# Kernel tuning notes

Hardware: AMD Instinct MI355X
Metric: run time of the kernel (lower is better)

## Reference

```python
import jax, jax.numpy as jnp
import numpy as np

D = 1024      # n_embedding
H = 16        # n_head
DH = D // H   # head_size = 64
T = 2048      # block_size / seq len
B = 2
EPS = 1e-5


def layer_norm(x, gamma, beta):
    mu = jnp.mean(x, axis=-1, keepdims=True)
    var = jnp.mean((x - mu) ** 2, axis=-1, keepdims=True)
    return (x - mu) * jax.lax.rsqrt(var + EPS) * gamma + beta


def setup_inputs() -> dict:
    key = jax.random.key(0)
    ks = jax.random.split(key, 12)
    s = 0.02
    return {
        "x": jax.random.normal(ks[0], (B, T, D), jnp.float32),
        # per-head QKV projections stacked over heads: [H, D, DH] (no bias, as in Head)
        "wq": jax.random.normal(ks[1], (H, D, DH), jnp.float32) * s,
        "wk": jax.random.normal(ks[2], (H, D, DH), jnp.float32) * s,
        "wv": jax.random.normal(ks[3], (H, D, DH), jnp.float32) * s,
        # output projection [H*DH, D] with bias
        "w_proj": jax.random.normal(ks[4], (H * DH, D), jnp.float32) * s,
        "b_proj": jnp.zeros((D,), jnp.float32),
        # feedforward: D -> 4D -> D
        "w1": jax.random.normal(ks[5], (D, 4 * D), jnp.float32) * s,
        "b1": jnp.zeros((4 * D,), jnp.float32),
        "w2": jax.random.normal(ks[6], (4 * D, D), jnp.float32) * s,
        "b2": jnp.zeros((D,), jnp.float32),
        # layer norms
        "ln1_g": jnp.ones((D,), jnp.float32),
        "ln1_b": jnp.zeros((D,), jnp.float32),
        "ln2_g": jnp.ones((D,), jnp.float32),
        "ln2_b": jnp.zeros((D,), jnp.float32),
    }


def reference(x, wq, wk, wv, w_proj, b_proj, w1, b1, w2, b2,
              ln1_g, ln1_b, ln2_g, ln2_b):
    # pre-LN attention sub-block
    xn = layer_norm(x, ln1_g, ln1_b)                      # [B,T,D]
    q = jnp.einsum('btd,hdk->bhtk', xn, wq)               # [B,H,T,DH]
    k = jnp.einsum('btd,hdk->bhtk', xn, wk)
    v = jnp.einsum('btd,hdk->bhtk', xn, wv)
    scale = DH ** -0.5
    scores = jnp.einsum('bhtk,bhsk->bhts', q, k) * scale  # [B,H,T,T]
    causal = jnp.tril(jnp.ones((T, T), bool))
    scores = jnp.where(causal, scores, -jnp.inf)
    attn = jax.nn.softmax(scores, axis=-1)
    out = jnp.einsum('bhts,bhsk->bhtk', attn, v)          # [B,H,T,DH]
    out = out.transpose(0, 2, 1, 3).reshape(B, T, H * DH)  # concat heads
    x = x + out @ w_proj + b_proj                          # residual 1
    # pre-LN feedforward sub-block
    xn2 = layer_norm(x, ln2_g, ln2_b)
    h = jax.nn.relu(xn2 @ w1 + b1)
    x = x + h @ w2 + b2                                    # residual 2
    return x
```

## Files before the change

### kernel.cpp

```cpp
#include <hip/hip_runtime.h>
#include <hip/hip_bf16.h>
#include <math.h>


#define D_MODEL 1024
#define NH 16
#define DHEAD 64
#define SEQ 2048
#define NTOK 4096

typedef __bf16 bf16x8 __attribute__((ext_vector_type(8)));
typedef float f32x4 __attribute__((ext_vector_type(4)));
typedef float f32x16 __attribute__((ext_vector_type(16)));
typedef unsigned short u16x8 __attribute__((ext_vector_type(8)));

__device__ __forceinline__ unsigned short f2b(float f) {
  unsigned u = __builtin_bit_cast(unsigned, f);
  u = u + 0x7fffu + ((u >> 16) & 1u);
  return (unsigned short)(u >> 16);
}

__device__ __forceinline__ bf16x8 ld_bf16x8(const unsigned short* p) {
  u16x8 u = *(const u16x8*)p;
  return __builtin_bit_cast(bf16x8, u);
}

__device__ __forceinline__ void async16(void* lds, const void* g) {
  __builtin_amdgcn_global_load_lds(
      (const __attribute__((address_space(1))) unsigned int*)g,
      (__attribute__((address_space(3))) unsigned int*)lds, 16, 0, 0);
}

__device__ __forceinline__ bf16x8 ds_read16(const void* p) {
  bf16x8 r;
  unsigned a = (unsigned)(size_t)(const __attribute__((address_space(3))) void*)p;
  asm volatile("ds_read_b128 %0, %1" : "=v"(r) : "v"(a));
  return r;
}
__device__ __forceinline__ void ds_write32(void* p, unsigned v) {
  unsigned a = (unsigned)(size_t)(__attribute__((address_space(3))) void*)p;
  asm volatile("ds_write_b32 %0, %1" :: "v"(a), "v"(v));
}
__device__ __forceinline__ unsigned cvt_pk_bf16(float lo, float hi) {
  unsigned d;
  asm("v_cvt_pk_bf16_f32 %0, %1, %2" : "=v"(d) : "v"(lo), "v"(hi));
  return d;
}
#define WAIT_LGKM0_FENCE() do { \
  asm volatile("s_waitcnt lgkmcnt(0)" ::: "memory"); \
  __builtin_amdgcn_sched_barrier(0); } while (0)
#define WAIT_LGKM8_FENCE() do { \
  asm volatile("s_waitcnt lgkmcnt(8)" ::: "memory"); \
  __builtin_amdgcn_sched_barrier(0); } while (0)

__global__ __launch_bounds__(256) void prep_fused(
    const float* __restrict__ wq, const float* __restrict__ wk,
    const float* __restrict__ wv, const float* __restrict__ w_proj,
    const float* __restrict__ w1, const float* __restrict__ w2,
    const float* __restrict__ x, const float* __restrict__ ln1g,
    const float* __restrict__ ln1b,
    unsigned short* __restrict__ WqkvT, unsigned short* __restrict__ wprojT,
    unsigned short* __restrict__ w1T, unsigned short* __restrict__ w2T,
    unsigned short* __restrict__ xn) {
  __shared__ float tile[64][65];
  __shared__ float ps[4], ps2[4];
  const int bid = blockIdx.x;
  const int tidx = threadIdx.x;

  if (bid < 3072) {
    const float* in;
    unsigned short* outp;
    int r0, c0, R, C;
    if (bid < 768) {
      int t = bid;
      int sel = t >> 8, hh = (t >> 4) & 15, rt = t & 15;
      in = (sel == 0 ? wq : sel == 1 ? wk : wv) + (size_t)hh * D_MODEL * DHEAD;
      int d0 = rt * 64;
      for (int i = 0; i < 16; i++) {
        int idx = i * 256 + tidx;
        int r = idx >> 6, c = idx & 63;
        tile[r][c] = in[(size_t)(d0 + r) * DHEAD + c];
      }
      __syncthreads();
      unsigned short* ob = WqkvT + (size_t)(sel * 1024 + hh * 64) * D_MODEL + d0;
      for (int i = 0; i < 16; i++) {
        int idx = i * 256 + tidx;
        int c = idx >> 6, r = idx & 63;
        ob[(size_t)c * D_MODEL + r] = f2b(tile[r][c]);
      }
      return;
    } else if (bid < 1024) {
      int t = bid - 768;
      in = w_proj; outp = wprojT; R = 1024; C = 1024;
      r0 = (t & 15) * 64; c0 = (t >> 4) * 64;
    } else if (bid < 2048) {
      int t = bid - 1024;
      in = w1; outp = w1T; R = 1024; C = 4096;
      r0 = (t & 15) * 64; c0 = (t >> 4) * 64;
    } else {
      int t = bid - 2048;
      in = w2; outp = w2T; R = 4096; C = 1024;
      r0 = (t & 63) * 64; c0 = (t >> 6) * 64;
    }
    for (int i = 0; i < 16; i++) {
      int idx = i * 256 + tidx;
      int r = idx >> 6, c = idx & 63;
      tile[r][c] = in[(size_t)(r0 + r) * C + c0 + c];
    }
    __syncthreads();
    for (int i = 0; i < 16; i++) {
      int idx = i * 256 + tidx;
      int c = idx >> 6, r = idx & 63;
      outp[(size_t)(c0 + c) * R + r0 + r] = f2b(tile[r][c]);
    }
    return;
  }

  const int row = bid - 3072;
  const float4* xr = (const float4*)(x + (size_t)row * D_MODEL);
  float4 v = xr[tidx];
  float s = v.x + v.y + v.z + v.w;
  float s2 = v.x * v.x + v.y * v.y + v.z * v.z + v.w * v.w;
  for (int m = 1; m < 64; m <<= 1) {
    s += __shfl_xor(s, m);
    s2 += __shfl_xor(s2, m);
  }
  int wid = tidx >> 6;
  if ((tidx & 63) == 0) { ps[wid] = s; ps2[wid] = s2; }
  __syncthreads();
  float S = ps[0] + ps[1] + ps[2] + ps[3];
  float S2 = ps2[0] + ps2[1] + ps2[2] + ps2[3];
  float mu = S * (1.f / D_MODEL);
  float var = S2 * (1.f / D_MODEL) - mu * mu;
  float inv = rsqrtf(var + 1e-5f);
  float4 gv = ((const float4*)ln1g)[tidx];
  float4 bv = ((const float4*)ln1b)[tidx];
  ushort4 o;
  o.x = f2b((v.x - mu) * inv * gv.x + bv.x);
  o.y = f2b((v.y - mu) * inv * gv.y + bv.y);
  o.z = f2b((v.z - mu) * inv * gv.z + bv.z);
  o.w = f2b((v.w - mu) * inv * gv.w + bv.w);
  ((ushort4*)(xn + (size_t)row * D_MODEL))[tidx] = o;
}

__global__ __launch_bounds__(256) void layernorm_bf16(
    const float* __restrict__ x, const float* __restrict__ g,
    const float* __restrict__ bta, unsigned short* __restrict__ out) {
  int row = blockIdx.x;
  int tid = threadIdx.x;
  const float4* xr = (const float4*)(x + (size_t)row * D_MODEL);
  float4 v = xr[tid];
  float s = v.x + v.y + v.z + v.w;
  float s2 = v.x * v.x + v.y * v.y + v.z * v.z + v.w * v.w;
  for (int m = 1; m < 64; m <<= 1) {
    s += __shfl_xor(s, m);
    s2 += __shfl_xor(s2, m);
  }
  __shared__ float ps[4], ps2[4];
  int wid = tid >> 6;
  if ((tid & 63) == 0) { ps[wid] = s; ps2[wid] = s2; }
  __syncthreads();
  float S = ps[0] + ps[1] + ps[2] + ps[3];
  float S2 = ps2[0] + ps2[1] + ps2[2] + ps2[3];
  float mu = S * (1.f / D_MODEL);
  float var = S2 * (1.f / D_MODEL) - mu * mu;
  float inv = rsqrtf(var + 1e-5f);
  float4 gv = ((const float4*)g)[tid];
  float4 bv = ((const float4*)bta)[tid];
  ushort4 o;
  o.x = f2b((v.x - mu) * inv * gv.x + bv.x);
  o.y = f2b((v.y - mu) * inv * gv.y + bv.y);
  o.z = f2b((v.z - mu) * inv * gv.z + bv.z);
  o.w = f2b((v.w - mu) * inv * gv.w + bv.w);
  ((ushort4*)(out + (size_t)row * D_MODEL))[tid] = o;
}

template <int TAG>
__global__ __launch_bounds__(256, 3) void gemm_n64(
    const unsigned short* __restrict__ A, const unsigned short* __restrict__ BT,
    int M, int N, int K,
    const float* __restrict__ bias, const float* __restrict__ resid,
    float* __restrict__ outF) {
  __shared__ alignas(16) unsigned short lsA[2][128 * 64];
  __shared__ alignas(16) unsigned short lsB[2][64 * 64];
  const int tid = threadIdx.x;
  const int wid = tid >> 6, lane = tid & 63;
  const int lr = lane & 15, lg = lane >> 4;
  const int row0 = blockIdx.x * 128, col0 = blockIdx.y * 64;
  const int wr = (wid >> 1) * 64, wc = (wid & 1) * 32;
  f32x4 acc[4][2] = {};
  const int nk = K >> 6;

  auto STAGE = [&](int bi, int kt) {
    const int k0 = kt << 6;
#pragma unroll
    for (int i = 0; i < 4; i++) {
      int sidx = i * 256 + tid;
      int r = sidx >> 3, s = sidx & 7;
      int ss = s ^ (r & 7);
      async16((char*)lsA[bi] + (i * 256 + wid * 64) * 16,
              A + (size_t)(row0 + r) * K + k0 + ss * 8);
    }
#pragma unroll
    for (int i = 0; i < 2; i++) {
      int sidx = i * 256 + tid;
      int r = sidx >> 3, s = sidx & 7;
      int ss = s ^ (r & 7);
      async16((char*)lsB[bi] + (i * 256 + wid * 64) * 16,
              BT + (size_t)(col0 + r) * K + k0 + ss * 8);
    }
  };

  STAGE(0, 0);
  for (int kt = 0; kt < nk; ++kt) {
    const int cur = kt & 1;
    if (kt + 1 < nk) {
      STAGE(cur ^ 1, kt + 1);
      asm volatile("s_waitcnt vmcnt(6)" ::: "memory");
    } else {
      asm volatile("s_waitcnt vmcnt(0)" ::: "memory");
    }
    __builtin_amdgcn_s_barrier();
    __builtin_amdgcn_sched_barrier(0);
#pragma unroll
    for (int kk = 0; kk < 2; ++kk) {
      bf16x8 af[4], bfr[2];
#pragma unroll
      for (int m = 0; m < 4; m++) {
        int r = wr + m * 16 + lr;
        int sw = (kk * 4 + lg) ^ (r & 7);
        af[m] = ds_read16((const char*)lsA[cur] + r * 128 + sw * 16);
      }
#pragma unroll
      for (int n = 0; n < 2; n++) {
        int r = wc + n * 16 + lr;
        int sw = (kk * 4 + lg) ^ (r & 7);
        bfr[n] = ds_read16((const char*)lsB[cur] + r * 128 + sw * 16);
      }
      WAIT_LGKM0_FENCE();
      __builtin_amdgcn_s_setprio(1);
#pragma unroll
      for (int m = 0; m < 4; m++)
#pragma unroll
        for (int n = 0; n < 2; n++)
          acc[m][n] = __builtin_amdgcn_mfma_f32_16x16x32_bf16(af[m], bfr[n], acc[m][n], 0, 0, 0);
      __builtin_amdgcn_s_setprio(0);
    }
    __builtin_amdgcn_sched_barrier(0);
    __builtin_amdgcn_s_barrier();
  }
#pragma unroll
  for (int m = 0; m < 4; m++) {
#pragma unroll
    for (int n = 0; n < 2; n++) {
#pragma unroll
      for (int r2 = 0; r2 < 4; r2++) {
        int row = row0 + wr + m * 16 + lg * 4 + r2;
        int col = col0 + wc + n * 16 + lr;
        float v = acc[m][n][r2] + bias[col] + resid[(size_t)row * N + col];
        outF[(size_t)row * N + col] = v;
      }
    }
  }
}

template <int MODE>
__global__ __launch_bounds__(512, 2) void gemm256_bt(
    const unsigned short* __restrict__ A, const unsigned short* __restrict__ BT,
    int M, int N, int K, int ntn,
    const float* __restrict__ bias, unsigned short* __restrict__ outB,
    unsigned short* __restrict__ outQ, unsigned short* __restrict__ outK,
    unsigned short* __restrict__ outV) {
  __shared__ alignas(16) unsigned short ls[2][2][2][256 * 32];
  const int tid = threadIdx.x;
  const int wid = tid >> 6, lane = tid & 63;
  const int lr = lane & 15, lg = lane >> 4;
  const int nwg = gridDim.x;
  const int wg = (blockIdx.x & 7) * (nwg >> 3) + (blockIdx.x >> 3);
  const int row0 = (wg / ntn) * 256, col0 = (wg % ntn) * 256;
  const int mbase = (wid >> 2) * 128;
  const int nbase = (wid & 3) * 64;

  f32x4 acc[8][4] = {};

  auto STAGE = [&](int buf, int kh, int ab, int kt) {
    const unsigned short* src = ab ? (BT + (size_t)col0 * K) : (A + (size_t)row0 * K);
    const int kbase = kt * 64 + kh * 32;
    unsigned short* dst0 = &ls[buf][kh][ab][0];
#pragma unroll
    for (int c = 0; c < 2; c++) {
      int s = c * 512 + tid;
      int row = s >> 2, c2 = s & 3;
      int ss = c2 ^ ((row >> 1) & 3);
      async16(dst0 + (size_t)(c * 512 + wid * 64) * 8,
              src + (size_t)row * K + kbase + ss * 8);
    }
  };
  auto LDA = [&](bf16x8* a, int buf, int kk, int mh) {
#pragma unroll
    for (int i = 0; i < 4; i++) {
      int mrow = mbase + (mh * 4 + i) * 16 + lr;
      int ch = lg ^ ((mrow >> 1) & 3);
      a[i] = ds_read16(&ls[buf][kk][0][mrow * 32 + ch * 8]);
    }
  };
  auto LDB = [&](bf16x8* b, int buf, int kk) {
#pragma unroll
    for (int i = 0; i < 4; i++) {
      int brow = nbase + i * 16 + lr;
      int ch = lg ^ ((brow >> 1) & 3);
      b[i] = ds_read16(&ls[buf][kk][1][brow * 32 + ch * 8]);
    }
  };

  const int nk = K >> 6;
  STAGE(0, 0, 0, 0); STAGE(0, 0, 1, 0); STAGE(0, 1, 0, 0); STAGE(0, 1, 1, 0);
  asm volatile("s_waitcnt vmcnt(4)" ::: "memory");
  __builtin_amdgcn_s_barrier();

  for (int t = 0; t < nk; ++t) {
    const int cur = t & 1, nxt = cur ^ 1;
    const bool haveNext = (t + 1 < nk);
    bf16x8 a[4], b[4];
    LDA(a, cur, 0, 0); LDB(b, cur, 0);
    if (haveNext) STAGE(nxt, 0, 0, t + 1);
    __builtin_amdgcn_s_barrier();
    WAIT_LGKM0_FENCE();
    __builtin_amdgcn_s_setprio(1);
#pragma unroll
    for (int i = 0; i < 4; i++)
#pragma unroll
      for (int j = 0; j < 4; j++)
        acc[i][j] = __builtin_amdgcn_mfma_f32_16x16x32_bf16(a[i], b[j], acc[i][j], 0, 0, 0);
    __builtin_amdgcn_s_setprio(0);
    __builtin_amdgcn_s_barrier();
    LDA(a, cur, 0, 1);
    if (haveNext) {
      STAGE(nxt, 0, 1, t + 1);
      asm volatile("s_waitcnt vmcnt(4)" ::: "memory");
    } else {
      asm volatile("s_waitcnt vmcnt(0)" ::: "memory");
    }
    __builtin_amdgcn_s_barrier();
    WAIT_LGKM0_FENCE();
    __builtin_amdgcn_s_setprio(1);
#pragma unroll
    for (int i = 0; i < 4; i++)
#pragma unroll
      for (int j = 0; j < 4; j++)
        acc[4 + i][j] = __builtin_amdgcn_mfma_f32_16x16x32_bf16(a[i], b[j], acc[4 + i][j], 0, 0, 0);
    __builtin_amdgcn_s_setprio(0);
    __builtin_amdgcn_s_barrier();
    LDA(a, cur, 1, 0); LDB(b, cur, 1);
    if (haveNext) STAGE(nxt, 1, 0, t + 1);
    __builtin_amdgcn_s_barrier();
    WAIT_LGKM0_FENCE();
    __builtin_amdgcn_s_setprio(1);
#pragma unroll
    for (int i = 0; i < 4; i++)
#pragma unroll
      for (int j = 0; j < 4; j++)
        acc[i][j] = __builtin_amdgcn_mfma_f32_16x16x32_bf16(a[i], b[j], acc[i][j], 0, 0, 0);
    __builtin_amdgcn_s_setprio(0);
    __builtin_amdgcn_s_barrier();
    LDA(a, cur, 1, 1);
    if (haveNext) {
      STAGE(nxt, 1, 1, t + 1);
      asm volatile("s_waitcnt vmcnt(4)" ::: "memory");
    }
    __builtin_amdgcn_s_barrier();
    WAIT_LGKM0_FENCE();
    __builtin_amdgcn_s_setprio(1);
#pragma unroll
    for (int i = 0; i < 4; i++)
#pragma unroll
      for (int j = 0; j < 4; j++)
        acc[4 + i][j] = __builtin_amdgcn_mfma_f32_16x16x32_bf16(a[i], b[j], acc[4 + i][j], 0, 0, 0);
    __builtin_amdgcn_s_setprio(0);
    __builtin_amdgcn_s_barrier();
  }
#pragma unroll
  for (int mi = 0; mi < 8; mi++) {
#pragma unroll
    for (int ni = 0; ni < 4; ni++) {
#pragma unroll
      for (int r2 = 0; r2 < 4; r2++) {
        int row = row0 + mbase + mi * 16 + lg * 4 + r2;
        int col = col0 + nbase + ni * 16 + lr;
        float v = acc[mi][ni][r2];
        if constexpr (MODE == 1) {
          v += bias[col];
          outB[(size_t)row * N + col] = f2b(fmaxf(v, 0.f));
        } else {
          int sel = col >> 10, jj = col & 1023, hh = jj >> 6, dh = jj & 63;
          int b2 = row >> 11, tt = row & 2047;
          size_t bh = (size_t)(b2 * NH + hh);
          if (sel == 0)      outQ[(bh * SEQ + tt) * DHEAD + dh] = f2b(v);
          else if (sel == 1) outK[(bh * SEQ + tt) * DHEAD + dh] = f2b(v);
          else               outV[(bh * DHEAD + dh) * SEQ + tt] = f2b(v);
        }
      }
    }
  }
}


#define ATTN_READS(KF, VF, G) do {                                          \
  int krow_ = 32 * (G) + l31;                                               \
  int ksw_ = krow_ & 7;                                                     \
  _Pragma("unroll")                                                         \
  for (int dk_ = 0; dk_ < 4; dk_++) {                                       \
    int ch_ = (2 * dk_ + h) ^ ksw_;                                         \
    KF[dk_] = ds_read16((const char*)Kc + krow_ * 128 + ch_ * 16);          \
  }                                                                         \
  _Pragma("unroll")                                                         \
  for (int dg_ = 0; dg_ < 2; dg_++) {                                       \
    int vrow_ = 32 * dg_ + l31;                                             \
    int vsw_ = vrow_ & 7;                                                   \
    _Pragma("unroll")                                                       \
    for (int c_ = 0; c_ < 2; c_++) {                                        \
      int kk_ = 2 * (G) + c_;                                               \
      int ch_ = (2 * kk_ + h) ^ vsw_;                                       \
      VF[dg_ * 2 + c_] = ds_read16((const char*)Vc + vrow_ * 256 + ch_ * 16); \
    }                                                                       \
  }                                                                         \
} while (0)

#define ATTN_COMPUTE(KF, VF, G, OA, OB) do {                                \
  const int s0g_ = s0 + 32 * (G);                                           \
  const bool needMask_ = (s0g_ == q0w);                                     \
  f32x16 st_ = {};                                                          \
  _Pragma("unroll")                                                         \
  for (int dk_ = 0; dk_ < 4; dk_++)                                         \
    st_ = __builtin_amdgcn_mfma_f32_32x32x16_bf16(KF[dk_], qf[dk_], st_, 0, 0, 0); \
  float p_[16];                                                             \
  _Pragma("unroll")                                                         \
  for (int reg_ = 0; reg_ < 16; reg_++) {                                   \
    float xx_ = st_[reg_] * cs;                                             \
    if (needMask_) {                                                        \
      int kg_ = s0g_ + (reg_ & 3) + 8 * (reg_ >> 2) + 4 * h;                \
      if (kg_ > q0w + l31) xx_ = -INFINITY;                                 \
    }                                                                       \
    float e_ = __builtin_amdgcn_exp2f(xx_);                                 \
    p_[reg_] = e_;                                                          \
    psum4[reg_ & 3] += e_;                                                  \
  }                                                                         \
  unsigned w_[8];                                                           \
  _Pragma("unroll")                                                         \
  for (int s_ = 0; s_ < 4; s_++) {                                          \
    w_[s_ * 2 + 0] = cvt_pk_bf16(p_[s_ * 4 + 0], p_[s_ * 4 + 1]);           \
    w_[s_ * 2 + 1] = cvt_pk_bf16(p_[s_ * 4 + 2], p_[s_ * 4 + 3]);           \
  }                                                                         \
  _Pragma("unroll")                                                         \
  for (int c_ = 0; c_ < 2; c_++) {                                          \
    unsigned a0_ = w_[(2 * c_) * 2 + 0], b0_ = w_[(2 * c_ + 1) * 2 + 0];    \
    unsigned a1_ = w_[(2 * c_) * 2 + 1], b1_ = w_[(2 * c_ + 1) * 2 + 1];    \
    asm volatile("v_permlane32_swap_b32 %0, %1" : "+v"(a0_), "+v"(b0_));    \
    asm volatile("v_permlane32_swap_b32 %0, %1" : "+v"(a1_), "+v"(b1_));    \
    uint4 pw_ = {a0_, a1_, b0_, b1_};                                       \
    bf16x8 pf_ = __builtin_bit_cast(bf16x8, pw_);                           \
    OA = __builtin_amdgcn_mfma_f32_32x32x16_bf16(VF[0 * 2 + c_], pf_, OA, 0, 0, 0); \
    OB = __builtin_amdgcn_mfma_f32_32x32x16_bf16(VF[1 * 2 + c_], pf_, OB, 0, 0, 0); \
  }                                                                         \
} while (0)

__global__ __launch_bounds__(256, 2) void attn_fwd(
    const unsigned short* __restrict__ Q, const unsigned short* __restrict__ K,
    const unsigned short* __restrict__ VT, unsigned short* __restrict__ O) {
  __shared__ alignas(16) unsigned short Kl[2][8192];
  __shared__ alignas(16) unsigned short Vl[2][8192];
  const int tid = threadIdx.x, wid = tid >> 6, lane = tid & 63;
  const int l31 = lane & 31, h = lane >> 5;
  const int xcd = (int)(blockIdx.x & 7), u = (int)(blockIdx.x >> 3);
  const int slot = u >> 5, v = u & 31;
  const int idx = xcd * 32 + v;
  const int bh = idx >> 3;
  const int qt = slot ? (7 - (idx & 7)) : (8 + (idx & 7));
  const unsigned short* Qb = Q + (size_t)bh * SEQ * DHEAD;
  const unsigned short* Kb = K + (size_t)bh * SEQ * DHEAD;
  const unsigned short* Vb = VT + (size_t)bh * DHEAD * SEQ;
  const int q0w = qt * 128 + wid * 32;
  bf16x8 qf[4];
#pragma unroll
  for (int dk = 0; dk < 4; dk++)
    qf[dk] = ld_bf16x8(Qb + (size_t)(q0w + l31) * DHEAD + dk * 16 + h * 8);
  f32x16 o0a = {}, o1a = {}, o0b = {}, o1b = {};
  float psum4[4] = {0.f, 0.f, 0.f, 0.f};
  const float cs = 0.18033688011112042f;
  const int nsteps = qt + 1;

  auto STAGE = [&](unsigned short* Kd, unsigned short* Vd, int s0) {
#pragma unroll
    for (int c = 0; c < 4; c++) {
      int s = c * 256 + tid;
      int row = s >> 3, sl = s & 7;
      int ss = sl ^ (row & 7);
      async16((char*)Kd + (c * 256 + wid * 64) * 16,
              Kb + (size_t)(s0 + row) * DHEAD + ss * 8);
    }
#pragma unroll
    for (int c = 0; c < 4; c++) {
      int s = c * 256 + tid;
      int row = s >> 4, sl = s & 15;
      int ss = sl ^ (row & 7);
      async16((char*)Vd + (c * 256 + wid * 64) * 16,
              Vb + (size_t)row * SEQ + s0 + ss * 8);
    }
  };

  STAGE(Kl[0], Vl[0], 0);
  for (int t = 0; t < nsteps; ++t) {
    if (t + 1 < nsteps) {
      STAGE(Kl[(t + 1) & 1], Vl[(t + 1) & 1], (t + 1) * 128);
      asm volatile("s_waitcnt vmcnt(8)" ::: "memory");
    } else {
      asm volatile("s_waitcnt vmcnt(0)" ::: "memory");
    }
    __builtin_amdgcn_s_barrier();
    __builtin_amdgcn_sched_barrier(0);
    const unsigned short* Kc = Kl[t & 1];
    const unsigned short* Vc = Vl[t & 1];
    const int s0 = t * 128;
    const int ng = (s0 <= q0w) ? ((q0w - s0) >> 5) >= 3 ? 4 : (((q0w - s0) >> 5) + 1) : 0;
    if (ng > 0) {
      bf16x8 kfA[4], vfA[4], kfB[4], vfB[4];
      ATTN_READS(kfA, vfA, 0);
      if (ng > 1) { ATTN_READS(kfB, vfB, 1); WAIT_LGKM8_FENCE(); }
      else        { WAIT_LGKM0_FENCE(); }
      ATTN_COMPUTE(kfA, vfA, 0, o0a, o1a);
      if (ng > 1) {
        if (ng > 2) { ATTN_READS(kfA, vfA, 2); WAIT_LGKM8_FENCE(); }
        else        { WAIT_LGKM0_FENCE(); }
        ATTN_COMPUTE(kfB, vfB, 1, o0b, o1b);
        if (ng > 2) {
          if (ng > 3) { ATTN_READS(kfB, vfB, 3); WAIT_LGKM8_FENCE(); }
          else        { WAIT_LGKM0_FENCE(); }
          ATTN_COMPUTE(kfA, vfA, 2, o0a, o1a);
          if (ng > 3) {
            WAIT_LGKM0_FENCE();
            ATTN_COMPUTE(kfB, vfB, 3, o0b, o1b);
          }
        }
      }
    }
    __builtin_amdgcn_sched_barrier(0);
    __builtin_amdgcn_s_barrier();
  }
  f32x16 o0 = o0a + o0b, o1 = o1a + o1b;
  float psum = (psum4[0] + psum4[1]) + (psum4[2] + psum4[3]);
  psum += __shfl_xor(psum, 32);
  float inv = 1.f / psum;
  unsigned short* slice = (unsigned short*)Kl + wid * 2048;
#pragma unroll
  for (int dg = 0; dg < 2; dg++) {
#pragma unroll
    for (int s = 0; s < 4; s++) {
#pragma unroll
      for (int m = 0; m < 2; m++) {
        float va = (dg ? o1[s * 4 + 2 * m] : o0[s * 4 + 2 * m]) * inv;
        float vb = (dg ? o1[s * 4 + 2 * m + 1] : o0[s * 4 + 2 * m + 1]) * inv;
        unsigned wv = cvt_pk_bf16(va, vb);
        int d = 32 * dg + 8 * s + 4 * h + 2 * m;
        ds_write32(&slice[l31 * 64 + d], wv);
      }
    }
  }
  WAIT_LGKM0_FENCE();
  bf16x8 ov[4];
#pragma unroll
  for (int pss = 0; pss < 4; pss++) {
    int qrow = pss * 8 + (lane >> 3);
    int d0 = (lane & 7) * 8;
    ov[pss] = ds_read16(&slice[qrow * 64 + d0]);
  }
  WAIT_LGKM0_FENCE();
  const int b = bh >> 4, head = bh & 15;
#pragma unroll
  for (int pss = 0; pss < 4; pss++) {
    int qrow = pss * 8 + (lane >> 3);
    int d0 = (lane & 7) * 8;
    *(bf16x8*)(O + ((size_t)b * SEQ + q0w + qrow) * D_MODEL + head * DHEAD + d0) = ov[pss];
  }
}


extern "C" void kernel_launch(void* const* d_in, const int* in_sizes, int n_in,
                              void* d_out, int out_size, void* d_ws, size_t ws_size,
                              hipStream_t stream) {
  const float* x = (const float*)d_in[0];
  const float* wq = (const float*)d_in[1];
  const float* wk = (const float*)d_in[2];
  const float* wv = (const float*)d_in[3];
  const float* w_proj = (const float*)d_in[4];
  const float* b_proj = (const float*)d_in[5];
  const float* w1 = (const float*)d_in[6];
  const float* b1 = (const float*)d_in[7];
  const float* w2 = (const float*)d_in[8];
  const float* b2 = (const float*)d_in[9];
  const float* ln1g = (const float*)d_in[10];
  const float* ln1b = (const float*)d_in[11];
  const float* ln2g = (const float*)d_in[12];
  const float* ln2b = (const float*)d_in[13];

  char* ws = (char*)d_ws;
  const size_t MB = 1024ull * 1024ull;
  unsigned short* xn = (unsigned short*)(ws + 0);
  unsigned short* Qb = (unsigned short*)(ws + 8 * MB);
  unsigned short* Kb = (unsigned short*)(ws + 16 * MB);
  unsigned short* VTb = (unsigned short*)(ws + 24 * MB);
  unsigned short* aout = (unsigned short*)(ws + 32 * MB);
  unsigned short* hbuf = (unsigned short*)(ws + 40 * MB);
  unsigned short* WqkvT = (unsigned short*)(ws + 72 * MB);
  unsigned short* wprojT = (unsigned short*)(ws + 78 * MB);
  unsigned short* w1T = (unsigned short*)(ws + 80 * MB);
  unsigned short* w2T = (unsigned short*)(ws + 88 * MB);
  float* x1 = (float*)d_out;

  prep_fused<<<dim3(7168), 256, 0, stream>>>(
      wq, wk, wv, w_proj, w1, w2, x, ln1g, ln1b,
      WqkvT, wprojT, w1T, w2T, xn);
  gemm256_bt<2><<<dim3(192), 512, 0, stream>>>(xn, WqkvT, NTOK, 3072, 1024, 12,
      nullptr, nullptr, Qb, Kb, VTb);
  attn_fwd<<<dim3(512), 256, 0, stream>>>(Qb, Kb, VTb, aout);
  gemm_n64<0><<<dim3(32, 16), 256, 0, stream>>>(aout, wprojT, NTOK, 1024, 1024,
      b_proj, x, x1);
  layernorm_bf16<<<NTOK, 256, 0, stream>>>(x1, ln2g, ln2b, xn);
  gemm256_bt<1><<<dim3(256), 512, 0, stream>>>(xn, w1T, NTOK, 4096, 1024, 16,
      b1, hbuf, nullptr, nullptr, nullptr);
  gemm_n64<1><<<dim3(32, 16), 256, 0, stream>>>(hbuf, w2T, NTOK, 1024, 4096,
      b2, x1, (float*)d_out);
}
```

Before: 223.0 us.

## Write QKV GEMM output row-major and transpose V in a separate kernel

The QKV projection GEMM now writes a plain row-major [tokens, 3072] bf16 buffer, replacing its scattered per-head Q/K/V stores and the strided transposed V store. A new small kernel transposes the V slice through shared memory into the per-head V^T layout. The attention kernel reads Q and K straight from the combined buffer with a 3072-element row stride. The aim is to remove the uncoalesced scatter epilogue, at the cost of an extra launch and another pass over V, plus strided Q/K loads in attention.

```diff
diff --git a/kernel.cpp b/kernel.cpp
--- a/kernel.cpp
+++ b/kernel.cpp
@@ -8,6 +8,7 @@
 #define DHEAD 64
 #define SEQ 2048
 #define NTOK 4096
+#define QKV_LD 3072
 
 typedef __bf16 bf16x8 __attribute__((ext_vector_type(8)));
 typedef float f32x4 __attribute__((ext_vector_type(4)));
@@ -175,6 +176,28 @@
   ((ushort4*)(out + (size_t)row * D_MODEL))[tid] = o;
 }
 
+__global__ __launch_bounds__(256) void vtrans(
+    const unsigned short* __restrict__ QKVc, unsigned short* __restrict__ VT) {
+  __shared__ unsigned short tile[64][72];
+  const int tt = blockIdx.x;
+  const int bh = blockIdx.y;
+  const int b = bh >> 4, hh = bh & 15;
+  const unsigned short* in = QKVc + ((size_t)b * SEQ + tt * 64) * QKV_LD
+                             + 2048 + hh * 64;
+  unsigned short* out = VT + (size_t)bh * DHEAD * SEQ + tt * 64;
+  for (int i = 0; i < 16; i++) {
+    int idx = i * 256 + threadIdx.x;
+    int r = idx >> 6, c = idx & 63;
+    tile[r][c] = in[(size_t)r * QKV_LD + c];
+  }
+  __syncthreads();
+  for (int i = 0; i < 16; i++) {
+    int idx = i * 256 + threadIdx.x;
+    int c = idx >> 6, r = idx & 63;
+    out[(size_t)c * SEQ + r] = tile[r][c];
+  }
+}
+
 template <int TAG>
 __global__ __launch_bounds__(256, 3) void gemm_n64(
     const unsigned short* __restrict__ A, const unsigned short* __restrict__ BT,
@@ -264,13 +287,10 @@
   }
 }
 
-template <int MODE>
 __global__ __launch_bounds__(512, 2) void gemm256_bt(
     const unsigned short* __restrict__ A, const unsigned short* __restrict__ BT,
     int M, int N, int K, int ntn,
-    const float* __restrict__ bias, unsigned short* __restrict__ outB,
-    unsigned short* __restrict__ outQ, unsigned short* __restrict__ outK,
-    unsigned short* __restrict__ outV) {
+    const float* __restrict__ bias, unsigned short* __restrict__ outB) {
   __shared__ alignas(16) unsigned short ls[2][2][2][256 * 32];
   const int tid = threadIdx.x;
   const int wid = tid >> 6, lane = tid & 63;
@@ -387,18 +407,134 @@
       for (int r2 = 0; r2 < 4; r2++) {
         int row = row0 + mbase + mi * 16 + lg * 4 + r2;
         int col = col0 + nbase + ni * 16 + lr;
-        float v = acc[mi][ni][r2];
-        if constexpr (MODE == 1) {
-          v += bias[col];
-          outB[(size_t)row * N + col] = f2b(fmaxf(v, 0.f));
-        } else {
-          int sel = col >> 10, jj = col & 1023, hh = jj >> 6, dh = jj & 63;
-          int b2 = row >> 11, tt = row & 2047;
-          size_t bh = (size_t)(b2 * NH + hh);
-          if (sel == 0)      outQ[(bh * SEQ + tt) * DHEAD + dh] = f2b(v);
-          else if (sel == 1) outK[(bh * SEQ + tt) * DHEAD + dh] = f2b(v);
-          else               outV[(bh * DHEAD + dh) * SEQ + tt] = f2b(v);
-        }
+        float v = acc[mi][ni][r2] + bias[col];
+        outB[(size_t)row * N + col] = f2b(fmaxf(v, 0.f));
+      }
+    }
+  }
+}
+
+__global__ __launch_bounds__(512, 2) void gemm256_c(
+    const unsigned short* __restrict__ A, const unsigned short* __restrict__ BT,
+    int M, int N, int K, int ntn,
+    unsigned short* __restrict__ outB) {
+  __shared__ alignas(16) unsigned short ls[2][2][2][256 * 32];
+  const int tid = threadIdx.x;
+  const int wid = tid >> 6, lane = tid & 63;
+  const int lr = lane & 15, lg = lane >> 4;
+  const int nwg = gridDim.x;
+  const int wg = (blockIdx.x & 7) * (nwg >> 3) + (blockIdx.x >> 3);
+  const int row0 = (wg / ntn) * 256, col0 = (wg % ntn) * 256;
+  const int mbase = (wid >> 2) * 128;
+  const int nbase = (wid & 3) * 64;
+
+  f32x4 acc[8][4] = {};
+
+  auto STAGE = [&](int buf, int kh, int ab, int kt) {
+    const unsigned short* src = ab ? (BT + (size_t)col0 * K) : (A + (size_t)row0 * K);
+    const int kbase = kt * 64 + kh * 32;
+    unsigned short* dst0 = &ls[buf][kh][ab][0];
+#pragma unroll
+    for (int c = 0; c < 2; c++) {
+      int s = c * 512 + tid;
+      int row = s >> 2, c2 = s & 3;
+      int ss = c2 ^ ((row >> 1) & 3);
+      async16(dst0 + (size_t)(c * 512 + wid * 64) * 8,
+              src + (size_t)row * K + kbase + ss * 8);
+    }
+  };
+  auto LDA = [&](bf16x8* a, int buf, int kk, int mh) {
+#pragma unroll
+    for (int i = 0; i < 4; i++) {
+      int mrow = mbase + (mh * 4 + i) * 16 + lr;
+      int ch = lg ^ ((mrow >> 1) & 3);
+      a[i] = ds_read16(&ls[buf][kk][0][mrow * 32 + ch * 8]);
+    }
+  };
+  auto LDB = [&](bf16x8* b, int buf, int kk) {
+#pragma unroll
+    for (int i = 0; i < 4; i++) {
+      int brow = nbase + i * 16 + lr;
+      int ch = lg ^ ((brow >> 1) & 3);
+      b[i] = ds_read16(&ls[buf][kk][1][brow * 32 + ch * 8]);
+    }
+  };
+
+  const int nk = K >> 6;
+  STAGE(0, 0, 0, 0); STAGE(0, 0, 1, 0); STAGE(0, 1, 0, 0); STAGE(0, 1, 1, 0);
+  asm volatile("s_waitcnt vmcnt(4)" ::: "memory");
+  __builtin_amdgcn_s_barrier();
+
+  for (int t = 0; t < nk; ++t) {
+    const int cur = t & 1, nxt = cur ^ 1;
+    const bool haveNext = (t + 1 < nk);
+    bf16x8 a[4], b[4];
+    LDA(a, cur, 0, 0); LDB(b, cur, 0);
+    if (haveNext) STAGE(nxt, 0, 0, t + 1);
+    __builtin_amdgcn_s_barrier();
+    WAIT_LGKM0_FENCE();
+    __builtin_amdgcn_s_setprio(1);
+#pragma unroll
+    for (int i = 0; i < 4; i++)
+#pragma unroll
+      for (int j = 0; j < 4; j++)
+        acc[i][j] = __builtin_amdgcn_mfma_f32_16x16x32_bf16(a[i], b[j], acc[i][j], 0, 0, 0);
+    __builtin_amdgcn_s_setprio(0);
+    __builtin_amdgcn_s_barrier();
+    LDA(a, cur, 0, 1);
+    if (haveNext) {
+      STAGE(nxt, 0, 1, t + 1);
+      asm volatile("s_waitcnt vmcnt(4)" ::: "memory");
+    } else {
+      asm volatile("s_waitcnt vmcnt(0)" ::: "memory");
+    }
+    __builtin_amdgcn_s_barrier();
+    WAIT_LGKM0_FENCE();
+    __builtin_amdgcn_s_setprio(1);
+#pragma unroll
+    for (int i = 0; i < 4; i++)
+#pragma unroll
+      for (int j = 0; j < 4; j++)
+        acc[4 + i][j] = __builtin_amdgcn_mfma_f32_16x16x32_bf16(a[i], b[j], acc[4 + i][j], 0, 0, 0);
+    __builtin_amdgcn_s_setprio(0);
+    __builtin_amdgcn_s_barrier();
+    LDA(a, cur, 1, 0); LDB(b, cur, 1);
+    if (haveNext) STAGE(nxt, 1, 0, t + 1);
+    __builtin_amdgcn_s_barrier();
+    WAIT_LGKM0_FENCE();
+    __builtin_amdgcn_s_setprio(1);
+#pragma unroll
+    for (int i = 0; i < 4; i++)
+#pragma unroll
+      for (int j = 0; j < 4; j++)
+        acc[i][j] = __builtin_amdgcn_mfma_f32_16x16x32_bf16(a[i], b[j], acc[i][j], 0, 0, 0);
+    __builtin_amdgcn_s_setprio(0);
+    __builtin_amdgcn_s_barrier();
+    LDA(a, cur, 1, 1);
+    if (haveNext) {
+      STAGE(nxt, 1, 1, t + 1);
+      asm volatile("s_waitcnt vmcnt(4)" ::: "memory");
+    }
+    __builtin_amdgcn_s_barrier();
+    WAIT_LGKM0_FENCE();
+    __builtin_amdgcn_s_setprio(1);
+#pragma unroll
+    for (int i = 0; i < 4; i++)
+#pragma unroll
+      for (int j = 0; j < 4; j++)
+        acc[4 + i][j] = __builtin_amdgcn_mfma_f32_16x16x32_bf16(a[i], b[j], acc[4 + i][j], 0, 0, 0);
+    __builtin_amdgcn_s_setprio(0);
+    __builtin_amdgcn_s_barrier();
+  }
+#pragma unroll
+  for (int mi = 0; mi < 8; mi++) {
+#pragma unroll
+    for (int ni = 0; ni < 4; ni++) {
+#pragma unroll
+      for (int r2 = 0; r2 < 4; r2++) {
+        int row = row0 + mbase + mi * 16 + lg * 4 + r2;
+        int col = col0 + nbase + ni * 16 + lr;
+        outB[(size_t)row * N + col] = f2b(acc[mi][ni][r2]);
       }
     }
   }
@@ -465,8 +601,8 @@
 } while (0)
 
 __global__ __launch_bounds__(256, 2) void attn_fwd(
-    const unsigned short* __restrict__ Q, const unsigned short* __restrict__ K,
-    const unsigned short* __restrict__ VT, unsigned short* __restrict__ O) {
+    const unsigned short* __restrict__ QKVc, const unsigned short* __restrict__ VT,
+    unsigned short* __restrict__ O) {
   __shared__ alignas(16) unsigned short Kl[2][8192];
   __shared__ alignas(16) unsigned short Vl[2][8192];
   const int tid = threadIdx.x, wid = tid >> 6, lane = tid & 63;
@@ -476,14 +612,15 @@
   const int idx = xcd * 32 + v;
   const int bh = idx >> 3;
   const int qt = slot ? (7 - (idx & 7)) : (8 + (idx & 7));
-  const unsigned short* Qb = Q + (size_t)bh * SEQ * DHEAD;
-  const unsigned short* Kb = K + (size_t)bh * SEQ * DHEAD;
+  const int b = bh >> 4, hh = bh & 15;
+  const unsigned short* Qb = QKVc + (size_t)b * SEQ * QKV_LD + hh * 64;
+  const unsigned short* Kb = QKVc + (size_t)b * SEQ * QKV_LD + 1024 + hh * 64;
   const unsigned short* Vb = VT + (size_t)bh * DHEAD * SEQ;
   const int q0w = qt * 128 + wid * 32;
   bf16x8 qf[4];
 #pragma unroll
   for (int dk = 0; dk < 4; dk++)
-    qf[dk] = ld_bf16x8(Qb + (size_t)(q0w + l31) * DHEAD + dk * 16 + h * 8);
+    qf[dk] = ld_bf16x8(Qb + (size_t)(q0w + l31) * QKV_LD + dk * 16 + h * 8);
   f32x16 o0a = {}, o1a = {}, o0b = {}, o1b = {};
   float psum4[4] = {0.f, 0.f, 0.f, 0.f};
   const float cs = 0.18033688011112042f;
@@ -496,7 +633,7 @@
       int row = s >> 3, sl = s & 7;
       int ss = sl ^ (row & 7);
       async16((char*)Kd + (c * 256 + wid * 64) * 16,
-              Kb + (size_t)(s0 + row) * DHEAD + ss * 8);
+              Kb + (size_t)(s0 + row) * QKV_LD + ss * 8);
     }
 #pragma unroll
     for (int c = 0; c < 4; c++) {
@@ -574,12 +711,11 @@
     ov[pss] = ds_read16(&slice[qrow * 64 + d0]);
   }
   WAIT_LGKM0_FENCE();
-  const int b = bh >> 4, head = bh & 15;
 #pragma unroll
   for (int pss = 0; pss < 4; pss++) {
     int qrow = pss * 8 + (lane >> 3);
     int d0 = (lane & 7) * 8;
-    *(bf16x8*)(O + ((size_t)b * SEQ + q0w + qrow) * D_MODEL + head * DHEAD + d0) = ov[pss];
+    *(bf16x8*)(O + ((size_t)b * SEQ + q0w + qrow) * D_MODEL + hh * DHEAD + d0) = ov[pss];
   }
 }
 
@@ -605,11 +741,10 @@
   char* ws = (char*)d_ws;
   const size_t MB = 1024ull * 1024ull;
   unsigned short* xn = (unsigned short*)(ws + 0);
-  unsigned short* Qb = (unsigned short*)(ws + 8 * MB);
-  unsigned short* Kb = (unsigned short*)(ws + 16 * MB);
-  unsigned short* VTb = (unsigned short*)(ws + 24 * MB);
-  unsigned short* aout = (unsigned short*)(ws + 32 * MB);
-  unsigned short* hbuf = (unsigned short*)(ws + 40 * MB);
+  unsigned short* QKVc = (unsigned short*)(ws + 8 * MB);
+  unsigned short* VTb = (unsigned short*)(ws + 32 * MB);
+  unsigned short* aout = (unsigned short*)(ws + 40 * MB);
+  unsigned short* hbuf = (unsigned short*)(ws + 8 * MB);
   unsigned short* WqkvT = (unsigned short*)(ws + 72 * MB);
   unsigned short* wprojT = (unsigned short*)(ws + 78 * MB);
   unsigned short* w1T = (unsigned short*)(ws + 80 * MB);
@@ -619,14 +754,15 @@
   prep_fused<<<dim3(7168), 256, 0, stream>>>(
       wq, wk, wv, w_proj, w1, w2, x, ln1g, ln1b,
       WqkvT, wprojT, w1T, w2T, xn);
-  gemm256_bt<2><<<dim3(192), 512, 0, stream>>>(xn, WqkvT, NTOK, 3072, 1024, 12,
-      nullptr, nullptr, Qb, Kb, VTb);
-  attn_fwd<<<dim3(512), 256, 0, stream>>>(Qb, Kb, VTb, aout);
+  gemm256_c<<<dim3(192), 512, 0, stream>>>(xn, WqkvT, NTOK, 3072, 1024, 12,
+      QKVc);
+  vtrans<<<dim3(32, 32), 256, 0, stream>>>(QKVc, VTb);
+  attn_fwd<<<dim3(512), 256, 0, stream>>>(QKVc, VTb, aout);
   gemm_n64<0><<<dim3(32, 16), 256, 0, stream>>>(aout, wprojT, NTOK, 1024, 1024,
       b_proj, x, x1);
   layernorm_bf16<<<NTOK, 256, 0, stream>>>(x1, ln2g, ln2b, xn);
-  gemm256_bt<1><<<dim3(256), 512, 0, stream>>>(xn, w1T, NTOK, 4096, 1024, 16,
-      b1, hbuf, nullptr, nullptr, nullptr);
+  gemm256_bt<<<dim3(256), 512, 0, stream>>>(xn, w1T, NTOK, 4096, 1024, 16,
+      b1, hbuf);
   gemm_n64<1><<<dim3(32, 16), 256, 0, stream>>>(hbuf, w2T, NTOK, 1024, 4096,
       b2, x1, (float*)d_out);
 }
```

New measurement: 206.2 us. -7.6%, faster.
